# Optimization experiments

Measured on AMD Instinct MI355X. Metric: run time of the kernel, lower is better.

The kernel has to match this reference:

```python
import jax, jax.numpy as jnp
import numpy as np

# Module hyperparameters (init_kwargs): shape_data = [n_t, n_y, n_x]
N_T, N_Y, N_X = 5, 32, 32
N = N_Y * N_X            # nb_nodes
DX = DY = DT = 1.0


def setup_inputs() -> dict:
    key = jax.random.key(0)
    k1, k2, k3 = jax.random.split(key, 3)
    n_b = 4
    kappa = jax.random.uniform(k1, (n_b, 1, N, N_T), dtype=jnp.float32)
    m = jax.random.normal(k2, (n_b, 2, N, N_T), dtype=jnp.float32)
    H = jax.random.normal(k3, (n_b, 2, 2, N, N_T), dtype=jnp.float32)
    return {"kappa": kappa, "m": m, "H": H}


def _stencil_indices():
    # 9-point stencil on the n_y x n_x grid; row-major node index = y*n_x + x.
    yy, xx = np.meshgrid(np.arange(N_Y), np.arange(N_X), indexing="ij")
    yy, xx = yy.reshape(-1), xx.reshape(-1)
    node = np.arange(N)
    offs = [(0, 0), (0, 1), (0, -1), (1, 0), (-1, 0), (1, 1), (1, -1), (-1, 1), (-1, -1)]
    rows, cols, valid = [], [], []
    for oy, ox in offs:
        ny, nx = yy + oy, xx + ox
        ok = (ny >= 0) & (ny < N_Y) & (nx >= 0) & (nx < N_X)
        rows.append(node)
        cols.append(np.where(ok, ny * N_X + nx, node))
        valid.append(ok.astype(np.float32))
    return (jnp.asarray(np.concatenate(rows)),
            jnp.asarray(np.concatenate(cols)),
            jnp.asarray(np.concatenate(valid)))

ROWS, COLS, VALID = _stencil_indices()


def _build_A(kappa, m, H):
    # Finite-difference discretization of A = kappa^2 I + m.grad - div(H grad)
    # kappa: [b,t,N]; m: [b,t,2,N]; H: [b,t,2,2,N]
    mx, my = m[..., 0, :], m[..., 1, :]
    H11, H22 = H[..., 0, 0, :], H[..., 1, 1, :]
    H12 = 0.5 * (H[..., 0, 1, :] + H[..., 1, 0, :])
    c0 = kappa ** 2 + 2.0 * H11 / DX ** 2 + 2.0 * H22 / DY ** 2   # center
    cpx = mx / (2 * DX) - H11 / DX ** 2                           # (0,+1)
    cmx = -mx / (2 * DX) - H11 / DX ** 2                          # (0,-1)
    cpy = my / (2 * DY) - H22 / DY ** 2                           # (+1,0)
    cmy = -my / (2 * DY) - H22 / DY ** 2                          # (-1,0)
    cc = H12 / (2 * DX * DY)                                      # cross term
    # order matches _stencil_indices offsets
    vals = jnp.concatenate([c0, cpx, cmx, cpy, cmy, -cc, cc, cc, -cc], axis=-1)
    vals = vals * VALID                                           # zero out-of-grid neighbors
    b, t = vals.shape[0], vals.shape[1]
    A = jnp.zeros((b, t, N, N), vals.dtype)
    return A.at[:, :, ROWS, COLS].add(vals)


def reference(kappa, m, H):
    # rearrange to [batch, time, ...] leading
    kap = jnp.transpose(kappa[:, 0], (0, 2, 1))          # [b,t,N]
    mm = jnp.transpose(m, (0, 3, 1, 2))                  # [b,t,2,N]
    HH = jnp.transpose(H, (0, 4, 1, 2, 3))               # [b,t,2,2,N]
    A = _build_A(kap, mm, HH)                            # [b,t,N,N]
    I = jnp.eye(N, dtype=A.dtype)
    M = I + DT * A                                       # M_k = Id + dt * A_k
    MM = jnp.einsum("btij,btjk->btik", M, M)             # spspmm(M_k, M_k)
    b = M.shape[0]
    Q = jnp.zeros((b, N_T * N, N_T * N), A.dtype)
    # block-tridiagonal precision matrix assembly (QR = Id)
    Q = Q.at[:, 0:N, 0:N].set(MM[:, 0])
    Q = Q.at[:, 0:N, N:2 * N].set(-M[:, 1])
    for i in range(1, N_T - 1):
        Q = Q.at[:, i * N:(i + 1) * N, (i - 1) * N:i * N].set(-M[:, i - 1])
        Q = Q.at[:, i * N:(i + 1) * N, i * N:(i + 1) * N].set(MM[:, i] + I)
        Q = Q.at[:, i * N:(i + 1) * N, (i + 1) * N:(i + 2) * N].set(-M[:, i + 1])
    i = N_T - 1
    Q = Q.at[:, i * N:(i + 1) * N, (i - 1) * N:i * N].set(-M[:, i - 1])
    Q = Q.at[:, i * N:(i + 1) * N, i * N:(i + 1) * N].set(MM[:, i])
    return Q
```

## Files before the change

### kernel.cpp

```cpp
#include <hip/hip_runtime.h>

#define NT   5
#define NY   32
#define NX   32
#define NN   1024
#define QDIM 5120
#define NB   4

typedef float vfloat4 __attribute__((ext_vector_type(4)));

__device__ const int c_oy[9] = {0, 0, 0, 1, -1, 1, 1, -1, -1};
__device__ const int c_ox[9] = {0, 1, -1, 0, 0, 1, -1, 1, -1};

__device__ __forceinline__ void stencil9(const float* __restrict__ kap,
                                         const float* __restrict__ m,
                                         const float* __restrict__ H,
                                         int b, int t, int n, float s[9]) {
    float k   = kap[((size_t)b * NN + n) * NT + t];
    float mx  = m[(((size_t)b * 2 + 0) * NN + n) * NT + t];
    float my  = m[(((size_t)b * 2 + 1) * NN + n) * NT + t];
    float H11 = H[((((size_t)b * 2 + 0) * 2 + 0) * NN + n) * NT + t];
    float H01 = H[((((size_t)b * 2 + 0) * 2 + 1) * NN + n) * NT + t];
    float H10 = H[((((size_t)b * 2 + 1) * 2 + 0) * NN + n) * NT + t];
    float H22 = H[((((size_t)b * 2 + 1) * 2 + 1) * NN + n) * NT + t];
    float cc = 0.25f * (H01 + H10);
    s[0] = 1.0f + k * k + 2.0f * H11 + 2.0f * H22;
    s[1] =  0.5f * mx - H11;
    s[2] = -0.5f * mx - H11;
    s[3] =  0.5f * my - H22;
    s[4] = -0.5f * my - H22;
    s[5] = -cc;
    s[6] =  cc;
    s[7] =  cc;
    s[8] = -cc;
    int y = n >> 5, x = n & 31;
    if (x == NX - 1) { s[1] = 0.f; s[5] = 0.f; s[7] = 0.f; }
    if (x == 0)      { s[2] = 0.f; s[6] = 0.f; s[8] = 0.f; }
    if (y == NY - 1) { s[3] = 0.f; s[5] = 0.f; s[6] = 0.f; }
    if (y == 0)      { s[4] = 0.f; s[7] = 0.f; s[8] = 0.f; }
}

__global__ __launch_bounds__(256) void spde_fused(const float* __restrict__ kap,
                                                  const float* __restrict__ m,
                                                  const float* __restrict__ H,
                                                  float* __restrict__ Q) {
    const int oy[9] = {0, 0, 0, 1, -1, 1, 1, -1, -1};
    const int ox[9] = {0, 1, -1, 0, 0, 1, -1, 1, -1};

    int row = blockIdx.x;
    int b = row / (NT * NN);
    int g = row - b * (NT * NN);
    int t = g >> 10;
    int r = g & (NN - 1);
    int ry = r >> 5, rx = r & 31;
    int tid = threadIdx.x;

    __shared__ float lds_row[3][NN];
    __shared__ float sk[9][9];
    __shared__ float moff[2][9];

    {
        vfloat4 z4 = {0.f, 0.f, 0.f, 0.f};
        vfloat4* p = (vfloat4*)&lds_row[0][0];
#pragma unroll
        for (int w = 0; w < 3; ++w) p[tid + 256 * w] = z4;
    }
    if (tid < 9) {
        int ky = ry + c_oy[tid], kx = rx + c_ox[tid];
        bool valid = ((unsigned)ky < NY) && ((unsigned)kx < NX);
        int k = valid ? (ky * NX + kx) : r;
        float s[9];
        stencil9(kap, m, H, b, t, k, s);
#pragma unroll
        for (int e = 0; e < 9; ++e)
            sk[tid][(oy[e] + 1) * 3 + (ox[e] + 1)] = s[e];
    } else if (tid == 9) {
        float s[9] = {0,0,0,0,0,0,0,0,0};
        if (t >= 1) stencil9(kap, m, H, b, t - 1, r, s);
#pragma unroll
        for (int e = 0; e < 9; ++e) moff[0][e] = -s[e];
    } else if (tid == 10) {
        float s[9] = {0,0,0,0,0,0,0,0,0};
        if (t <= NT - 2) stencil9(kap, m, H, b, t + 1, r, s);
#pragma unroll
        for (int e = 0; e < 9; ++e) moff[1][e] = -s[e];
    }
    __syncthreads();

    if (tid < 25) {
        int dy = tid / 5 - 2, dx = tid % 5 - 2;
        float a = 0.f;
#pragma unroll
        for (int d1 = 0; d1 < 9; ++d1) {
            int dy2 = dy - oy[d1], dx2 = dx - ox[d1];
            if (dy2 >= -1 && dy2 <= 1 && dx2 >= -1 && dx2 <= 1) {
                a += sk[0][(oy[d1] + 1) * 3 + (ox[d1] + 1)]
                   * sk[d1][(dy2 + 1) * 3 + (dx2 + 1)];
            }
        }
        if (tid == 12 && t >= 1 && t <= NT - 2) a += 1.0f;
        int cy = ry + dy, cx = rx + dx;
        if ((unsigned)cy < NY && (unsigned)cx < NX)
            lds_row[1][cy * NX + cx] = a;
    } else if (tid >= 32 && tid < 41) {
        if (t >= 1) {
            int d = tid - 32;
            int cy = ry + c_oy[d], cx = rx + c_ox[d];
            if ((unsigned)cy < NY && (unsigned)cx < NX)
                lds_row[0][cy * NX + cx] = moff[0][d];
        }
    } else if (tid >= 48 && tid < 57) {
        if (t <= NT - 2) {
            int d = tid - 48;
            int cy = ry + c_oy[d], cx = rx + c_ox[d];
            if ((unsigned)cy < NY && (unsigned)cx < NX)
                lds_row[2][cy * NX + cx] = moff[1][d];
        }
    }
    __syncthreads();

    float* dst = Q + ((size_t)b * QDIM + g) * QDIM + 4 * tid;
    const vfloat4* src = (const vfloat4*)&lds_row[0][4 * tid];
    vfloat4 z4 = {0.f, 0.f, 0.f, 0.f};
#pragma unroll
    for (int kk = 0; kk < NT; ++kk) {
        int z = kk - t + 1;
        vfloat4 v = ((unsigned)z < 3u) ? src[(size_t)z * (NN / 4)] : z4;
        __builtin_nontemporal_store(v, (vfloat4*)(dst + (size_t)kk * NN));
    }
}

extern "C" void kernel_launch(void* const* d_in, const int* in_sizes, int n_in,
                              void* d_out, int out_size, void* d_ws, size_t ws_size,
                              hipStream_t stream) {
    const float* kap = (const float*)d_in[0];
    const float* m   = (const float*)d_in[1];
    const float* H   = (const float*)d_in[2];
    float* Q = (float*)d_out;

    int nrows = NB * NT * NN;
    spde_fused<<<nrows, 256, 0, stream>>>(kap, m, H, Q);
}
```

Baseline: 412.2 us.

## Split into stencil/product precompute kernel and a streaming write kernel

Adds a first kernel, one block per (batch, time) slice, that loads the coefficient planes into shared memory, builds every node's 9-point stencil and its 25-entry M*M product, and writes both to workspace. The streaming kernel then only reads precomputed records per row instead of recomputing 11 stencils with strided global loads. This removes redundant per-row arithmetic and scattered loads. In exchange it adds a second launch, a dependency between the kernels, and a build kernel with only 20 blocks that may serialize.

```diff
diff --git a/kernel.cpp b/kernel.cpp
--- a/kernel.cpp
+++ b/kernel.cpp
@@ -7,46 +7,102 @@
 #define QDIM 5120
 #define NB   4
 
+#define REC1 12
+#define REC2 28
+
 typedef float vfloat4 __attribute__((ext_vector_type(4)));
 
 __device__ const int c_oy[9] = {0, 0, 0, 1, -1, 1, 1, -1, -1};
 __device__ const int c_ox[9] = {0, 1, -1, 0, 0, 1, -1, 1, -1};
 
-__device__ __forceinline__ void stencil9(const float* __restrict__ kap,
-                                         const float* __restrict__ m,
-                                         const float* __restrict__ H,
-                                         int b, int t, int n, float s[9]) {
-    float k   = kap[((size_t)b * NN + n) * NT + t];
-    float mx  = m[(((size_t)b * 2 + 0) * NN + n) * NT + t];
-    float my  = m[(((size_t)b * 2 + 1) * NN + n) * NT + t];
-    float H11 = H[((((size_t)b * 2 + 0) * 2 + 0) * NN + n) * NT + t];
-    float H01 = H[((((size_t)b * 2 + 0) * 2 + 1) * NN + n) * NT + t];
-    float H10 = H[((((size_t)b * 2 + 1) * 2 + 0) * NN + n) * NT + t];
-    float H22 = H[((((size_t)b * 2 + 1) * 2 + 1) * NN + n) * NT + t];
-    float cc = 0.25f * (H01 + H10);
-    s[0] = 1.0f + k * k + 2.0f * H11 + 2.0f * H22;
-    s[1] =  0.5f * mx - H11;
-    s[2] = -0.5f * mx - H11;
-    s[3] =  0.5f * my - H22;
-    s[4] = -0.5f * my - H22;
-    s[5] = -cc;
-    s[6] =  cc;
-    s[7] =  cc;
-    s[8] = -cc;
-    int y = n >> 5, x = n & 31;
-    if (x == NX - 1) { s[1] = 0.f; s[5] = 0.f; s[7] = 0.f; }
-    if (x == 0)      { s[2] = 0.f; s[6] = 0.f; s[8] = 0.f; }
-    if (y == NY - 1) { s[3] = 0.f; s[5] = 0.f; s[6] = 0.f; }
-    if (y == 0)      { s[4] = 0.f; s[7] = 0.f; s[8] = 0.f; }
-}
-
-__global__ __launch_bounds__(256) void spde_fused(const float* __restrict__ kap,
+__global__ __launch_bounds__(256) void spde_build(const float* __restrict__ kap,
                                                   const float* __restrict__ m,
                                                   const float* __restrict__ H,
-                                                  float* __restrict__ Q) {
+                                                  float* __restrict__ W1,
+                                                  float* __restrict__ W2) {
     const int oy[9] = {0, 0, 0, 1, -1, 1, 1, -1, -1};
     const int ox[9] = {0, 1, -1, 0, 0, 1, -1, 1, -1};
 
+    int bt = blockIdx.x;
+    int t = bt % NT;
+    int b = bt / NT;
+    int tid = threadIdx.x;
+
+    __shared__ float pl[7][NN];
+    __shared__ float st[NN * 13];
+
+    const float* srcs[7] = {
+        kap + ((size_t)b * NN) * NT + t,
+        m   + ((size_t)(b * 2 + 0) * NN) * NT + t,
+        m   + ((size_t)(b * 2 + 1) * NN) * NT + t,
+        H   + ((size_t)((b * 2 + 0) * 2 + 0) * NN) * NT + t,
+        H   + ((size_t)((b * 2 + 0) * 2 + 1) * NN) * NT + t,
+        H   + ((size_t)((b * 2 + 1) * 2 + 0) * NN) * NT + t,
+        H   + ((size_t)((b * 2 + 1) * 2 + 1) * NN) * NT + t,
+    };
+#pragma unroll
+    for (int p = 0; p < 7; ++p)
+#pragma unroll
+        for (int w = 0; w < 4; ++w) {
+            int n = tid + 256 * w;
+            pl[p][n] = srcs[p][(size_t)n * NT];
+        }
+    __syncthreads();
+
+#pragma unroll
+    for (int w = 0; w < 4; ++w) {
+        int n = tid + 256 * w;
+        float k   = pl[0][n], mx = pl[1][n], my = pl[2][n];
+        float H11 = pl[3][n], H01 = pl[4][n], H10 = pl[5][n], H22 = pl[6][n];
+        float cc = 0.25f * (H01 + H10);
+        float s[9];
+        s[0] = 1.0f + k * k + 2.0f * H11 + 2.0f * H22;
+        s[1] =  0.5f * mx - H11;
+        s[2] = -0.5f * mx - H11;
+        s[3] =  0.5f * my - H22;
+        s[4] = -0.5f * my - H22;
+        s[5] = -cc; s[6] = cc; s[7] = cc; s[8] = -cc;
+        int y = n >> 5, x = n & 31;
+        if (x == NX - 1) { s[1] = 0.f; s[5] = 0.f; s[7] = 0.f; }
+        if (x == 0)      { s[2] = 0.f; s[6] = 0.f; s[8] = 0.f; }
+        if (y == NY - 1) { s[3] = 0.f; s[5] = 0.f; s[6] = 0.f; }
+        if (y == 0)      { s[4] = 0.f; s[7] = 0.f; s[8] = 0.f; }
+#pragma unroll
+        for (int e = 0; e < 9; ++e) st[n * 13 + e] = s[e];
+        float* o1 = W1 + ((size_t)bt * NN + n) * REC1;
+#pragma unroll
+        for (int e = 0; e < 9; ++e) o1[e] = s[e];
+    }
+    __syncthreads();
+
+#pragma unroll
+    for (int w = 0; w < 4; ++w) {
+        int n = tid + 256 * w;
+        int ry = n >> 5, rx = n & 31;
+        float acc[25];
+#pragma unroll
+        for (int e = 0; e < 25; ++e) acc[e] = 0.f;
+#pragma unroll
+        for (int d1 = 0; d1 < 9; ++d1) {
+            float a = st[n * 13 + d1];
+            int ky = ry + oy[d1], kx = rx + ox[d1];
+            bool valid = ((unsigned)ky < NY) && ((unsigned)kx < NX);
+            int k = valid ? (ky * NX + kx) : n;
+#pragma unroll
+            for (int d2 = 0; d2 < 9; ++d2)
+                acc[(oy[d1] + oy[d2] + 2) * 5 + (ox[d1] + ox[d2] + 2)]
+                    += a * st[k * 13 + d2];
+        }
+        if (t >= 1 && t <= NT - 2) acc[12] += 1.0f;
+        float* o2 = W2 + ((size_t)bt * NN + n) * REC2;
+#pragma unroll
+        for (int e = 0; e < 25; ++e) o2[e] = acc[e];
+    }
+}
+
+__global__ __launch_bounds__(256) void spde_stream(const float* __restrict__ W1,
+                                                   const float* __restrict__ W2,
+                                                   float* __restrict__ Q) {
     int row = blockIdx.x;
     int b = row / (NT * NN);
     int g = row - b * (NT * NN);
@@ -55,78 +111,52 @@
     int ry = r >> 5, rx = r & 31;
     int tid = threadIdx.x;
 
-    __shared__ float lds_row[3][NN];
-    __shared__ float sk[9][9];
-    __shared__ float moff[2][9];
+    __shared__ float img[3][NN];
 
+    vfloat4 z4 = {0.f, 0.f, 0.f, 0.f};
     {
-        vfloat4 z4 = {0.f, 0.f, 0.f, 0.f};
-        vfloat4* p = (vfloat4*)&lds_row[0][0];
+        vfloat4* p = (vfloat4*)&img[0][0];
 #pragma unroll
         for (int w = 0; w < 3; ++w) p[tid + 256 * w] = z4;
     }
-    if (tid < 9) {
-        int ky = ry + c_oy[tid], kx = rx + c_ox[tid];
-        bool valid = ((unsigned)ky < NY) && ((unsigned)kx < NX);
-        int k = valid ? (ky * NX + kx) : r;
-        float s[9];
-        stencil9(kap, m, H, b, t, k, s);
-#pragma unroll
-        for (int e = 0; e < 9; ++e)
-            sk[tid][(oy[e] + 1) * 3 + (ox[e] + 1)] = s[e];
-    } else if (tid == 9) {
-        float s[9] = {0,0,0,0,0,0,0,0,0};
-        if (t >= 1) stencil9(kap, m, H, b, t - 1, r, s);
-#pragma unroll
-        for (int e = 0; e < 9; ++e) moff[0][e] = -s[e];
-    } else if (tid == 10) {
-        float s[9] = {0,0,0,0,0,0,0,0,0};
-        if (t <= NT - 2) stencil9(kap, m, H, b, t + 1, r, s);
-#pragma unroll
-        for (int e = 0; e < 9; ++e) moff[1][e] = -s[e];
-    }
-    __syncthreads();
 
+    float v = 0.f;
+    int dst_idx = 0;
+    bool have = false;
     if (tid < 25) {
+        v = W2[((size_t)(b * NT + t) * NN + r) * REC2 + tid];
         int dy = tid / 5 - 2, dx = tid % 5 - 2;
-        float a = 0.f;
-#pragma unroll
-        for (int d1 = 0; d1 < 9; ++d1) {
-            int dy2 = dy - oy[d1], dx2 = dx - ox[d1];
-            if (dy2 >= -1 && dy2 <= 1 && dx2 >= -1 && dx2 <= 1) {
-                a += sk[0][(oy[d1] + 1) * 3 + (ox[d1] + 1)]
-                   * sk[d1][(dy2 + 1) * 3 + (dx2 + 1)];
-            }
-        }
-        if (tid == 12 && t >= 1 && t <= NT - 2) a += 1.0f;
         int cy = ry + dy, cx = rx + dx;
-        if ((unsigned)cy < NY && (unsigned)cx < NX)
-            lds_row[1][cy * NX + cx] = a;
+        have = ((unsigned)cy < NY) && ((unsigned)cx < NX);
+        dst_idx = 1 * NN + cy * NX + cx;
     } else if (tid >= 32 && tid < 41) {
         if (t >= 1) {
             int d = tid - 32;
+            v = -W1[((size_t)(b * NT + t - 1) * NN + r) * REC1 + d];
             int cy = ry + c_oy[d], cx = rx + c_ox[d];
-            if ((unsigned)cy < NY && (unsigned)cx < NX)
-                lds_row[0][cy * NX + cx] = moff[0][d];
+            have = ((unsigned)cy < NY) && ((unsigned)cx < NX);
+            dst_idx = 0 * NN + cy * NX + cx;
         }
     } else if (tid >= 48 && tid < 57) {
         if (t <= NT - 2) {
             int d = tid - 48;
+            v = -W1[((size_t)(b * NT + t + 1) * NN + r) * REC1 + d];
             int cy = ry + c_oy[d], cx = rx + c_ox[d];
-            if ((unsigned)cy < NY && (unsigned)cx < NX)
-                lds_row[2][cy * NX + cx] = moff[1][d];
+            have = ((unsigned)cy < NY) && ((unsigned)cx < NX);
+            dst_idx = 2 * NN + cy * NX + cx;
         }
     }
     __syncthreads();
+    if (have) (&img[0][0])[dst_idx] = v;
+    __syncthreads();
 
     float* dst = Q + ((size_t)b * QDIM + g) * QDIM + 4 * tid;
-    const vfloat4* src = (const vfloat4*)&lds_row[0][4 * tid];
-    vfloat4 z4 = {0.f, 0.f, 0.f, 0.f};
+    const vfloat4* src = (const vfloat4*)&img[0][4 * tid];
 #pragma unroll
     for (int kk = 0; kk < NT; ++kk) {
         int z = kk - t + 1;
-        vfloat4 v = ((unsigned)z < 3u) ? src[(size_t)z * (NN / 4)] : z4;
-        __builtin_nontemporal_store(v, (vfloat4*)(dst + (size_t)kk * NN));
+        vfloat4 vv = ((unsigned)z < 3u) ? src[(size_t)z * (NN / 4)] : z4;
+        __builtin_nontemporal_store(vv, (vfloat4*)(dst + (size_t)kk * NN));
     }
 }
 
@@ -138,6 +168,9 @@
     const float* H   = (const float*)d_in[2];
     float* Q = (float*)d_out;
 
-    int nrows = NB * NT * NN;
-    spde_fused<<<nrows, 256, 0, stream>>>(kap, m, H, Q);
+    float* W1 = (float*)d_ws;
+    float* W2 = (float*)((char*)d_ws + (1 << 20));
+
+    spde_build<<<NB * NT, 256, 0, stream>>>(kap, m, H, W1, W2);
+    spde_stream<<<NB * NT * NN, 256, 0, stream>>>(W1, W2, Q);
 }
```

Result: slower. 420.9 us (+2.1%).
